# Kernel optimization log

Hardware: AMD Instinct MI355X
Metric: run time of the kernel (lower is better)

## Reference

```python
import jax, jax.numpy as jnp
import numpy as np
import math

N_NODES = 50000
N_EDGES = 800000
F_IN = 32
HID = 64


def _layernorm(x, g, b, eps=1e-5):
    mu = x.mean(-1, keepdims=True)
    var = ((x - mu) ** 2).mean(-1, keepdims=True)
    return (x - mu) / jnp.sqrt(var + eps) * g + b


def _tconv(x, src, dst, Wq, bq, Wk, bk, Wv, bv, Ws, heads):
    # PyG TransformerConv (concat=True, root_weight=True, bias=False on skip)
    N = x.shape[0]
    C = Wq.shape[1] // heads
    q = (x @ Wq + bq).reshape(N, heads, C)[dst]  # [E,H,C] gathered at targets
    k = (x @ Wk + bk).reshape(N, heads, C)[src]  # [E,H,C] gathered at sources
    v = (x @ Wv + bv).reshape(N, heads, C)[src]
    scores = (q * k).sum(-1) / math.sqrt(C)      # [E,H]
    m = jax.ops.segment_max(scores, dst, num_segments=N)   # [N,H]
    p = jnp.exp(scores - m[dst])
    denom = jax.ops.segment_sum(p, dst, num_segments=N)
    alpha = p / (denom[dst] + 1e-16)             # segment softmax over in-edges
    agg = jax.ops.segment_sum(v * alpha[..., None], dst, num_segments=N)
    return agg.reshape(N, heads * C) + x @ Ws    # + skip (no bias)


def setup_inputs() -> dict:
    key = jax.random.key(0)
    ks = iter(jax.random.split(key, 64))
    def rn(shape, s=0.1):
        return jax.random.normal(next(ks), shape, jnp.float32) * s
    inp = {
        "x": rn((N_NODES, F_IN), 1.0),
        "edge_index": jax.random.randint(next(ks), (2, N_EDGES), 0, N_NODES, dtype=jnp.int32),
        "ln0_g": jnp.ones((F_IN,), jnp.float32),
        "ln0_b": jnp.zeros((F_IN,), jnp.float32),
    }
    dims = [F_IN, HID, HID]
    for l in range(3):
        d = dims[l]
        inp[f"Wq{l}"] = rn((d, HID)); inp[f"bq{l}"] = rn((HID,), 0.05)
        inp[f"Wk{l}"] = rn((d, HID)); inp[f"bk{l}"] = rn((HID,), 0.05)
        inp[f"Wv{l}"] = rn((d, HID)); inp[f"bv{l}"] = rn((HID,), 0.05)
        inp[f"Ws{l}"] = rn((d, HID))
        inp[f"g{l}"] = jnp.ones((HID,), jnp.float32)
        inp[f"b{l}"] = jnp.zeros((HID,), jnp.float32)
    inp["Wr1"] = rn((HID, HID // 2)); inp["br1"] = jnp.zeros((HID // 2,), jnp.float32)
    inp["Wr2"] = rn((HID // 2, 1));   inp["br2"] = jnp.zeros((1,), jnp.float32)
    inp["Wt1"] = rn((HID, HID // 2)); inp["bt1"] = jnp.zeros((HID // 2,), jnp.float32)
    inp["Wt2"] = rn((HID // 2, 1));   inp["bt2"] = jnp.zeros((1,), jnp.float32)
    return inp


def reference(x, edge_index, ln0_g, ln0_b,
              Wq0, bq0, Wk0, bk0, Wv0, bv0, Ws0, g0, b0,
              Wq1, bq1, Wk1, bk1, Wv1, bv1, Ws1, g1, b1,
              Wq2, bq2, Wk2, bk2, Wv2, bv2, Ws2, g2, b2,
              Wr1, br1, Wr2, br2, Wt1, bt1, Wt2, bt2):
    src, dst = edge_index[0], edge_index[1]
    h = _layernorm(x, ln0_g, ln0_b)
    layers = [
        (Wq0, bq0, Wk0, bk0, Wv0, bv0, Ws0, g0, b0, 4),
        (Wq1, bq1, Wk1, bk1, Wv1, bv1, Ws1, g1, b1, 4),
        (Wq2, bq2, Wk2, bk2, Wv2, bv2, Ws2, g2, b2, 1),
    ]
    for i, (Wq, bq, Wk, bk, Wv, bv, Ws, g, b, heads) in enumerate(layers):
        x_res = h if h.shape[-1] == HID else None
        h = _tconv(h, src, dst, Wq, bq, Wk, bk, Wv, bv, Ws, heads)
        h = _layernorm(h, g, b)
        if x_res is not None and i > 0:
            h = h + 0.1 * x_res
        if i < len(layers) - 1:
            h = jax.nn.relu(h)  # dropout is identity in eval mode
    rtt = jax.nn.relu(h @ Wr1 + br1) @ Wr2 + br2      # [N,1]
    retrans = jax.nn.relu(h @ Wt1 + bt1) @ Wt2 + bt2  # [N,1]
    return jnp.concatenate([rtt, retrans], axis=1)    # [N,2]
```

## Files before the change

kernel.cpp:

```cpp
#include <hip/hip_runtime.h>
#include <hip/hip_bf16.h>
#include <hip/hip_fp16.h>
#include <math.h>

#define N_NODES 50000
#define N_EDGES 800000
#define HID 64
#define NBK 196
#define EPB 1024
#define SB  ((N_EDGES + EPB - 1) / EPB)
#define FLAT (NBK * SB)
#define SCAN_B ((FLAT + 255) / 256)

#define QKVS0_BLKS 3125
#define SCORE_BLKS ((N_EDGES * 4) / 256)

#define LN0_BLKS   6250
#define HIST_BLKS  SB
#define WP0_BLKS   32
#define WP12_BLKS  64
#define PREP_BLKS  (LN0_BLKS + HIST_BLKS + WP0_BLKS + 2 * WP12_BLKS)

typedef __attribute__((ext_vector_type(8))) short short8;
typedef __attribute__((ext_vector_type(4))) float float4v;
typedef __attribute__((ext_vector_type(2))) float float2v;

__device__ __forceinline__ unsigned short f32_to_bf16_rne(float f) {
    unsigned int u = __float_as_uint(f);
    unsigned int r = u + 0x7fffu + ((u >> 16) & 1u);
    return (unsigned short)(r >> 16);
}

__device__ __forceinline__ unsigned int f32_to_fp8_byte(float f) {
    return (unsigned int)__builtin_amdgcn_cvt_pk_fp8_f32(f, f, 0, false) & 0xffu;
}
template <bool HI>
__device__ __forceinline__ float2v fp8x2_to_f32(unsigned int w) {
    return __builtin_amdgcn_cvt_pk_f32_fp8((int)w, HI);
}
__device__ __forceinline__ float2 h2_to_f32(unsigned int w) {
    __half2 h = *reinterpret_cast<__half2*>(&w);
    return __half22float2(h);
}

__device__ __forceinline__ void ln0_body(int b, int t,
        const float* __restrict__ x, const float* __restrict__ g,
        const float* __restrict__ bb, float* __restrict__ h0) {
    int lane = t & 63;
    int n = b * 8 + (t >> 6) * 2 + (lane >> 5);
    int c = lane & 31;
    float v = x[n * 32 + c];
    float s = v;
    #pragma unroll
    for (int off = 1; off < 32; off <<= 1) s += __shfl_xor(s, off);
    float mu = s * (1.0f / 32.0f);
    float d = v - mu;
    float vs = d * d;
    #pragma unroll
    for (int off = 1; off < 32; off <<= 1) vs += __shfl_xor(vs, off);
    float var = vs * (1.0f / 32.0f);
    h0[n * 32 + c] = d * rsqrtf(var + 1e-5f) * g[c] + bb[c];
}

__device__ __forceinline__ void wprep_body(int idx, int KS,
        const float* __restrict__ Wq, const float* __restrict__ Wk,
        const float* __restrict__ Wv, const float* __restrict__ Ws,
        unsigned short* __restrict__ Wp) {
    int j = idx & 7;
    int lane = (idx >> 3) & 63;
    int ts = idx >> 9;
    int s = ts % KS;
    int tile = ts / KS;
    int which = tile >> 2;
    int slice = tile & 3;
    int k = s * 32 + ((lane >> 4) * 8) + j;
    int col = slice * 16 + (lane & 15);
    const float* W = (which == 0) ? Wq : (which == 1) ? Wk : (which == 2) ? Wv : Ws;
    Wp[idx] = f32_to_bf16_rne(W[k * 64 + col]);
}

__global__ __launch_bounds__(256) void prep_kernel(
        const float* __restrict__ x, const float* __restrict__ ln0g,
        const float* __restrict__ ln0b, float* __restrict__ h0,
        const int* __restrict__ dst, int* __restrict__ ghist,
        const float* __restrict__ Wq0, const float* __restrict__ Wk0,
        const float* __restrict__ Wv0, const float* __restrict__ Ws0,
        unsigned short* __restrict__ Wp0,
        const float* __restrict__ Wq1, const float* __restrict__ Wk1,
        const float* __restrict__ Wv1, const float* __restrict__ Ws1,
        unsigned short* __restrict__ Wp1,
        const float* __restrict__ Wq2, const float* __restrict__ Wk2,
        const float* __restrict__ Wv2, const float* __restrict__ Ws2,
        unsigned short* __restrict__ Wp2) {
    __shared__ int hist[NBK];
    int b = blockIdx.x;
    int t = threadIdx.x;
    if (b < LN0_BLKS) {
        ln0_body(b, t, x, ln0g, ln0b, h0);
    } else if (b < LN0_BLKS + HIST_BLKS) {
        int i = b - LN0_BLKS;
        for (int k = t; k < NBK; k += 256) hist[k] = 0;
        __syncthreads();
        int e0 = i * EPB;
        #pragma unroll
        for (int r = 0; r < EPB / 256; r++) {
            int e = e0 + r * 256 + t;
            if (e < N_EDGES) atomicAdd(&hist[dst[e] >> 8], 1);
        }
        __syncthreads();
        for (int k = t; k < NBK; k += 256) ghist[k * SB + i] = hist[k];
    } else if (b < LN0_BLKS + HIST_BLKS + WP0_BLKS) {
        int idx = (b - LN0_BLKS - HIST_BLKS) * 256 + t;
        wprep_body(idx, 1, Wq0, Wk0, Wv0, Ws0, Wp0);
    } else if (b < LN0_BLKS + HIST_BLKS + WP0_BLKS + WP12_BLKS) {
        int idx = (b - LN0_BLKS - HIST_BLKS - WP0_BLKS) * 256 + t;
        wprep_body(idx, 2, Wq1, Wk1, Wv1, Ws1, Wp1);
    } else {
        int idx = (b - LN0_BLKS - HIST_BLKS - WP0_BLKS - WP12_BLKS) * 256 + t;
        wprep_body(idx, 2, Wq2, Wk2, Wv2, Ws2, Wp2);
    }
}

__global__ void scan1_kernel(const int* __restrict__ ghist, int* __restrict__ csum) {
    int f = blockIdx.x * 256 + threadIdx.x;
    int v = (f < FLAT) ? ghist[f] : 0;
    #pragma unroll
    for (int off = 1; off < 64; off <<= 1) v += __shfl_xor(v, off);
    __shared__ int ws[4];
    if ((threadIdx.x & 63) == 0) ws[threadIdx.x >> 6] = v;
    __syncthreads();
    if (threadIdx.x == 0) csum[blockIdx.x] = ws[0] + ws[1] + ws[2] + ws[3];
}

__global__ void scan2_kernel(const int* __restrict__ csum, int* __restrict__ coff,
                             int* __restrict__ bbase, int* __restrict__ row_ptr) {
    int lane = threadIdx.x;
    int carry = 0;
    for (int base = 0; base < SCAN_B; base += 64) {
        int i = base + lane;
        int v = (i < SCAN_B) ? csum[i] : 0;
        int incl = v;
        #pragma unroll
        for (int off = 1; off < 64; off <<= 1) {
            int tt = __shfl_up(incl, off);
            if (lane >= off) incl += tt;
        }
        if (i < SCAN_B) coff[i] = carry + incl - v;
        carry += __shfl(incl, 63);
    }
    if (lane == 0) { bbase[NBK] = N_EDGES; row_ptr[N_NODES] = N_EDGES; }
}

__global__ void scan3_kernel(const int* __restrict__ ghist, const int* __restrict__ coff,
                             int* __restrict__ goff, int* __restrict__ bbase) {
    int f = blockIdx.x * 256 + threadIdx.x;
    int lane = threadIdx.x & 63;
    int w = threadIdx.x >> 6;
    int v = (f < FLAT) ? ghist[f] : 0;
    int incl = v;
    #pragma unroll
    for (int off = 1; off < 64; off <<= 1) {
        int tt = __shfl_up(incl, off);
        if (lane >= off) incl += tt;
    }
    __shared__ int ws[4];
    if (lane == 63) ws[w] = incl;
    __syncthreads();
    int woff = 0;
    #pragma unroll
    for (int k = 0; k < 4; k++) if (k < w) woff += ws[k];
    int excl = coff[blockIdx.x] + woff + incl - v;
    if (f < FLAT) {
        goff[f] = excl;
        if (f % SB == 0) bbase[f / SB] = excl;
    }
}

template <int D>
__device__ __forceinline__ void qkvs_body(int bid, int t,
        const float* __restrict__ h,
        const unsigned short* __restrict__ Wp,
        const float* __restrict__ bq, const float* __restrict__ bk,
        const float* __restrict__ bv, float scale,
        unsigned int* __restrict__ QS,
        unsigned int* __restrict__ K8, uint2* __restrict__ Vh) {
    constexpr int KS = D / 32;
    int lane = t & 63;
    int w = t >> 6;
    int n0 = bid * 16;
    int n16 = lane & 15;
    int quad = lane >> 4;
    int col = w * 16 + n16;

    short8 afrag[KS];
    #pragma unroll
    for (int s = 0; s < KS; s++) {
        const float* hp = &h[(n0 + n16) * D + s * 32 + quad * 8];
        float4 a0 = *(const float4*)hp;
        float4 a1 = *(const float4*)(hp + 4);
        short8 af;
        af[0] = (short)f32_to_bf16_rne(a0.x);
        af[1] = (short)f32_to_bf16_rne(a0.y);
        af[2] = (short)f32_to_bf16_rne(a0.z);
        af[3] = (short)f32_to_bf16_rne(a0.w);
        af[4] = (short)f32_to_bf16_rne(a1.x);
        af[5] = (short)f32_to_bf16_rne(a1.y);
        af[6] = (short)f32_to_bf16_rne(a1.z);
        af[7] = (short)f32_to_bf16_rne(a1.w);
        afrag[s] = af;
    }

    float4v accs[4];
    #pragma unroll
    for (int which = 0; which < 4; which++) {
        float4v acc = {0.0f, 0.0f, 0.0f, 0.0f};
        int tile = which * 4 + w;
        #pragma unroll
        for (int s = 0; s < KS; s++) {
            short8 bfrag = *(const short8*)&Wp[((tile * KS + s) * 64 + lane) * 8];
            acc = __builtin_amdgcn_mfma_f32_16x16x32_bf16(afrag[s], bfrag, acc, 0, 0, 0);
        }
        accs[which] = acc;
    }

    float bqc = bq[col], bkc = bk[col], bvc = bv[col];
    int j = n16 & 3;
    int mword = (col >> 2);

    #pragma unroll
    for (int r = 0; r < 4; r++) {
        int node = n0 + quad * 4 + r;
        unsigned int qw = f32_to_bf16_rne((accs[0][r] + bqc) * scale);
        unsigned int sw = f32_to_bf16_rne(accs[3][r]);
        QS[node * 64 + col] = (sw << 16) | qw;
        unsigned int ku = f32_to_fp8_byte(accs[1][r] + bkc) << (8 * j);
        ku |= __shfl_xor(ku, 1); ku |= __shfl_xor(ku, 2);
        unsigned int hb = (unsigned int)__half_as_ushort(__float2half_rn(accs[2][r] + bvc));
        unsigned int vx = (j < 2) ? (hb << (16 * j)) : 0u;
        unsigned int vy = (j >= 2) ? (hb << (16 * (j - 2))) : 0u;
        vx |= __shfl_xor(vx, 1); vx |= __shfl_xor(vx, 2);
        vy |= __shfl_xor(vy, 1); vy |= __shfl_xor(vy, 2);
        if (j == 0) {
            K8[node * 16 + mword] = ku;
            Vh[node * 16 + mword] = make_uint2(vx, vy);
        }
    }
}

template <int D>
__global__ __launch_bounds__(256) void qkvs_mfma_kernel(
        const float* __restrict__ h,
        const unsigned short* __restrict__ Wp,
        const float* __restrict__ bq, const float* __restrict__ bk,
        const float* __restrict__ bv, float scale,
        unsigned int* __restrict__ QS,
        unsigned int* __restrict__ K8, uint2* __restrict__ Vh) {
    qkvs_body<D>(blockIdx.x, threadIdx.x, h, Wp, bq, bk, bv, scale, QS, K8, Vh);
}

__global__ __launch_bounds__(256) void scatter_qkvs0_kernel(
        const int* __restrict__ src, const int* __restrict__ dst,
        const int* __restrict__ goff, int2* __restrict__ ebkt,
        const float* __restrict__ h, const unsigned short* __restrict__ Wp,
        const float* __restrict__ bq, const float* __restrict__ bk,
        const float* __restrict__ bv, float scale,
        unsigned int* __restrict__ QS,
        unsigned int* __restrict__ K8, uint2* __restrict__ Vh) {
    __shared__ int hist[NBK];
    int t = threadIdx.x;
    if (blockIdx.x < SB) {
        int i = blockIdx.x;
        for (int k = t; k < NBK; k += 256) hist[k] = 0;
        __syncthreads();
        int e0 = i * EPB;
        #pragma unroll
        for (int r = 0; r < EPB / 256; r++) {
            int e = e0 + r * 256 + t;
            if (e < N_EDGES) {
                int s = src[e], d = dst[e];
                int k = d >> 8;
                int rank = atomicAdd(&hist[k], 1);
                ebkt[goff[k * SB + i] + rank] = make_int2(s, d);
            }
        }
    } else {
        qkvs_body<32>(blockIdx.x - SB, t, h, Wp, bq, bk, bv, scale, QS, K8, Vh);
    }
}

__global__ __launch_bounds__(256) void bucket_build_kernel(
        const int2* __restrict__ ebkt, const int* __restrict__ bbase,
        int* __restrict__ row_ptr, int2* __restrict__ colb2) {
    __shared__ int ldeg[256];
    __shared__ int lcur[256];
    __shared__ int wsum[4];
    int b = blockIdx.x;
    int t = threadIdx.x;
    int cbase = bbase[b];
    int cnt = bbase[b + 1] - cbase;

    ldeg[t] = 0;
    __syncthreads();
    for (int i = t; i < cnt; i += 256) {
        int2 e = ebkt[cbase + i];
        atomicAdd(&ldeg[e.y & 255], 1);
    }
    __syncthreads();

    int lane = t & 63;
    int w = t >> 6;
    int v = ldeg[t];
    int incl = v;
    #pragma unroll
    for (int off = 1; off < 64; off <<= 1) {
        int tt = __shfl_up(incl, off);
        if (lane >= off) incl += tt;
    }
    if (lane == 63) wsum[w] = incl;
    __syncthreads();
    int woff = 0;
    #pragma unroll
    for (int k = 0; k < 4; k++) if (k < w) woff += wsum[k];
    int excl = woff + incl - v;

    int node = b * 256 + t;
    if (node < N_NODES) row_ptr[node] = cbase + excl;
    lcur[t] = excl;
    __syncthreads();

    for (int i = t; i < cnt; i += 256) {
        int2 e = ebkt[cbase + i];
        int r = atomicAdd(&lcur[e.y & 255], 1);
        colb2[cbase + r] = e;
    }
}

template <int HEADS>
__global__ __launch_bounds__(256) void score_kernel(
        const unsigned int* __restrict__ QS,
        const unsigned int* __restrict__ K8,
        const int2* __restrict__ colb2,
        float* __restrict__ p) {
    int gid = blockIdx.x * 256 + threadIdx.x;
    int e = gid >> 2;
    int slot = gid & 3;
    int2 ed = colb2[e];
    const unsigned int* qp = &QS[(size_t)ed.y * 64 + slot * 16];
    uint4 qa = *(const uint4*)qp;
    uint4 qb = *(const uint4*)(qp + 4);
    uint4 qc = *(const uint4*)(qp + 8);
    uint4 qd = *(const uint4*)(qp + 12);
    uint4 kw = *(const uint4*)&K8[(size_t)ed.x * 16 + slot * 4];

    float2v k0 = fp8x2_to_f32<false>(kw.x), k1 = fp8x2_to_f32<true>(kw.x);
    float2v k2 = fp8x2_to_f32<false>(kw.y), k3 = fp8x2_to_f32<true>(kw.y);
    float2v k4 = fp8x2_to_f32<false>(kw.z), k5 = fp8x2_to_f32<true>(kw.z);
    float2v k6 = fp8x2_to_f32<false>(kw.w), k7 = fp8x2_to_f32<true>(kw.w);

    float t;
    t =      __uint_as_float(qa.x << 16) * k0.x;
    t = fmaf(__uint_as_float(qa.y << 16), k0.y, t);
    t = fmaf(__uint_as_float(qa.z << 16), k1.x, t);
    t = fmaf(__uint_as_float(qa.w << 16), k1.y, t);
    t = fmaf(__uint_as_float(qb.x << 16), k2.x, t);
    t = fmaf(__uint_as_float(qb.y << 16), k2.y, t);
    t = fmaf(__uint_as_float(qb.z << 16), k3.x, t);
    t = fmaf(__uint_as_float(qb.w << 16), k3.y, t);
    t = fmaf(__uint_as_float(qc.x << 16), k4.x, t);
    t = fmaf(__uint_as_float(qc.y << 16), k4.y, t);
    t = fmaf(__uint_as_float(qc.z << 16), k5.x, t);
    t = fmaf(__uint_as_float(qc.w << 16), k5.y, t);
    t = fmaf(__uint_as_float(qd.x << 16), k6.x, t);
    t = fmaf(__uint_as_float(qd.y << 16), k6.y, t);
    t = fmaf(__uint_as_float(qd.z << 16), k7.x, t);
    t = fmaf(__uint_as_float(qd.w << 16), k7.y, t);

    if (HEADS == 1) {
        t += __shfl_xor(t, 1);
        t += __shfl_xor(t, 2);
    }
    float pv = __expf(t);
    if (HEADS == 4) {
        p[(size_t)e * 4 + slot] = pv;
    } else {
        if (slot == 0) p[e] = pv;
    }
}

template <int HEADS, bool RES, bool RELU, bool HEAD>
__global__ __launch_bounds__(256) void agg_kernel(
                           const unsigned int* __restrict__ QS,
                           const uint2* __restrict__ Vh,
                           const float* __restrict__ p,
                           const int2* __restrict__ colb2,
                           const int* __restrict__ row_ptr,
                           const float* __restrict__ g, const float* __restrict__ b,
                           const float* __restrict__ h_in, float* __restrict__ h_out,
                           const float* __restrict__ Wr1, const float* __restrict__ br1,
                           const float* __restrict__ Wr2, const float* __restrict__ br2,
                           const float* __restrict__ Wt1, const float* __restrict__ bt1,
                           const float* __restrict__ Wt2, const float* __restrict__ bt2,
                           float* __restrict__ out) {
    int lane = threadIdx.x & 63;
    int m = lane & 15;
    int grp = lane >> 4;
    int n = blockIdx.x * 4 + (threadIdx.x >> 6);
    int hsel = m >> 2;

    int beg = row_ptr[n], end = row_ptr[n + 1];

    float ssum = 0.0f;
    float acc0 = 0.0f, acc1 = 0.0f, acc2 = 0.0f, acc3 = 0.0f;

    for (int base = beg; base < end; base += 16) {
        #pragma unroll
        for (int c = 0; c < 4; c++) {
            int idx = base + c * 4 + grp;
            bool ok = idx < end;
            int s = 0;
            float pv = 0.0f;
            if (ok) {
                s = colb2[idx].x;
                pv = (HEADS == 4) ? p[(size_t)idx * 4 + hsel] : p[idx];
            }
            uint2 va = Vh[(size_t)s * 16 + m];
            float2 v0 = h2_to_f32(va.x), v1 = h2_to_f32(va.y);
            ssum += pv;
            acc0 = fmaf(pv, v0.x, acc0);
            acc1 = fmaf(pv, v0.y, acc1);
            acc2 = fmaf(pv, v1.x, acc2);
            acc3 = fmaf(pv, v1.y, acc3);
        }
    }

    #pragma unroll
    for (int off = 16; off < 64; off <<= 1) {
        ssum += __shfl_xor(ssum, off);
        acc0 += __shfl_xor(acc0, off);
        acc1 += __shfl_xor(acc1, off);
        acc2 += __shfl_xor(acc2, off);
        acc3 += __shfl_xor(acc3, off);
    }

    float inv = 1.0f / (ssum + 1e-16f);
    uint4 qsw = *(const uint4*)&QS[(size_t)n * 64 + 4 * m];
    float o0 = fmaf(acc0, inv, __uint_as_float(qsw.x & 0xffff0000u));
    float o1 = fmaf(acc1, inv, __uint_as_float(qsw.y & 0xffff0000u));
    float o2 = fmaf(acc2, inv, __uint_as_float(qsw.z & 0xffff0000u));
    float o3 = fmaf(acc3, inv, __uint_as_float(qsw.w & 0xffff0000u));

    float s = (o0 + o1) + (o2 + o3);
    #pragma unroll
    for (int off = 1; off < 16; off <<= 1) s += __shfl_xor(s, off);
    float mu = s * (1.0f / 64.0f);
    float d0 = o0 - mu, d1 = o1 - mu, d2 = o2 - mu, d3 = o3 - mu;
    float vs = (d0 * d0 + d1 * d1) + (d2 * d2 + d3 * d3);
    #pragma unroll
    for (int off = 1; off < 16; off <<= 1) vs += __shfl_xor(vs, off);
    float rstd = rsqrtf(vs * (1.0f / 64.0f) + 1e-5f);

    float4 gv = *(const float4*)&g[4 * m];
    float4 bv = *(const float4*)&b[4 * m];
    float y0 = d0 * rstd * gv.x + bv.x;
    float y1 = d1 * rstd * gv.y + bv.y;
    float y2 = d2 * rstd * gv.z + bv.z;
    float y3 = d3 * rstd * gv.w + bv.w;
    if (RES) {
        float4 rv = *(const float4*)&h_in[n * 64 + 4 * m];
        y0 = fmaf(0.1f, rv.x, y0);
        y1 = fmaf(0.1f, rv.y, y1);
        y2 = fmaf(0.1f, rv.z, y2);
        y3 = fmaf(0.1f, rv.w, y3);
    }
    if (RELU) {
        y0 = fmaxf(y0, 0.0f); y1 = fmaxf(y1, 0.0f);
        y2 = fmaxf(y2, 0.0f); y3 = fmaxf(y3, 0.0f);
    }

    if (!HEAD) {
        if (grp == 0) {
            float4 yv = make_float4(y0, y1, y2, y3);
            *(float4*)&h_out[n * 64 + 4 * m] = yv;
        }
    } else {
        __shared__ float sh[4][HID];
        int wave = threadIdx.x >> 6;
        if (grp == 0) {
            float4 yv = make_float4(y0, y1, y2, y3);
            *(float4*)&sh[wave][4 * m] = yv;
        }
        __syncthreads();
        int half = lane >> 5;
        int j = lane & 31;
        const float* W1 = half ? Wt1 : Wr1;
        const float* b1 = half ? bt1 : br1;
        const float* W2 = half ? Wt2 : Wr2;
        const float* b2v = half ? bt2 : br2;
        float a = b1[j];
        #pragma unroll 8
        for (int i = 0; i < 64; i++) a = fmaf(sh[wave][i], W1[i * 32 + j], a);
        a = fmaxf(a, 0.0f);
        float r = a * W2[j];
        #pragma unroll
        for (int off = 1; off < 32; off <<= 1) r += __shfl_xor(r, off);
        if (j == 0) out[n * 2 + half] = r + b2v[0];
    }
}

extern "C" void kernel_launch(void* const* d_in, const int* in_sizes, int n_in,
                              void* d_out, int out_size, void* d_ws, size_t ws_size,
                              hipStream_t stream) {
    const float* x    = (const float*)d_in[0];
    const int*   ei   = (const int*)d_in[1];
    const int*   src  = ei;
    const int*   dst  = ei + N_EDGES;
    const float* ln0g = (const float*)d_in[2];
    const float* ln0b = (const float*)d_in[3];

    const float* P[27];
    for (int i = 0; i < 27; i++) P[i] = (const float*)d_in[4 + i];
    const float* Wr1 = (const float*)d_in[31];
    const float* br1 = (const float*)d_in[32];
    const float* Wr2 = (const float*)d_in[33];
    const float* br2 = (const float*)d_in[34];
    const float* Wt1 = (const float*)d_in[35];
    const float* bt1 = (const float*)d_in[36];
    const float* Wt2 = (const float*)d_in[37];
    const float* bt2 = (const float*)d_in[38];

    float* out = (float*)d_out;

    float* hbuf0 = (float*)d_ws;
    float* hbuf1 = hbuf0 + N_NODES * 64;
    unsigned int* QSb = (unsigned int*)(hbuf1 + N_NODES * 64);
    unsigned int* K8 = QSb + N_NODES * 64;
    uint2* Vh    = (uint2*)(K8 + N_NODES * 16);
    float* pbuf  = (float*)(Vh + N_NODES * 16);
    int* row_ptr = (int*)(pbuf + (size_t)N_EDGES * 4);
    int2* colb2  = (int2*)(row_ptr + (N_NODES + 2));
    int* ghist   = (int*)(colb2 + N_EDGES);
    int* goff    = ghist + FLAT;
    int* csum    = goff + FLAT;
    int* coff    = csum + SCAN_B;
    int* bbase   = coff + SCAN_B;
    unsigned short* Wp0 = (unsigned short*)(bbase + NBK + 1);
    unsigned short* Wp1 = Wp0 + 16 * 1 * 512;
    unsigned short* Wp2 = Wp1 + 16 * 2 * 512;
    int2* ebkt = (int2*)hbuf1;

    prep_kernel<<<PREP_BLKS, 256, 0, stream>>>(x, ln0g, ln0b, hbuf0,
        dst, ghist,
        P[0],  P[2],  P[4],  P[6],  Wp0,
        P[9],  P[11], P[13], P[15], Wp1,
        P[18], P[20], P[22], P[24], Wp2);
    scan1_kernel<<<SCAN_B, 256, 0, stream>>>(ghist, csum);
    scan2_kernel<<<1, 64, 0, stream>>>(csum, coff, bbase, row_ptr);
    scan3_kernel<<<SCAN_B, 256, 0, stream>>>(ghist, coff, goff, bbase);
    scatter_qkvs0_kernel<<<SB + QKVS0_BLKS, 256, 0, stream>>>(src, dst, goff, ebkt,
        hbuf0, Wp0, P[1], P[3], P[5], 0.25f, QSb, K8, Vh);
    bucket_build_kernel<<<NBK, 256, 0, stream>>>(ebkt, bbase, row_ptr, colb2);

    score_kernel<4><<<SCORE_BLKS, 256, 0, stream>>>(QSb, K8, colb2, pbuf);
    agg_kernel<4, false, true, false><<<12500, 256, 0, stream>>>(QSb, Vh, pbuf,
        colb2, row_ptr, P[7], P[8], nullptr, hbuf1,
        Wr1, br1, Wr2, br2, Wt1, bt1, Wt2, bt2, out);

    qkvs_mfma_kernel<64><<<3125, 256, 0, stream>>>(hbuf1, Wp1,
        P[10], P[12], P[14], 0.25f, QSb, K8, Vh);
    score_kernel<4><<<SCORE_BLKS, 256, 0, stream>>>(QSb, K8, colb2, pbuf);
    agg_kernel<4, true, true, false><<<12500, 256, 0, stream>>>(QSb, Vh, pbuf,
        colb2, row_ptr, P[16], P[17], hbuf1, hbuf0,
        Wr1, br1, Wr2, br2, Wt1, bt1, Wt2, bt2, out);

    qkvs_mfma_kernel<64><<<3125, 256, 0, stream>>>(hbuf0, Wp2,
        P[19], P[21], P[23], 0.125f, QSb, K8, Vh);
    score_kernel<1><<<SCORE_BLKS, 256, 0, stream>>>(QSb, K8, colb2, pbuf);
    agg_kernel<1, true, false, true><<<12500, 256, 0, stream>>>(QSb, Vh, pbuf,
        colb2, row_ptr, P[25], P[26], hbuf0, hbuf1,
        Wr1, br1, Wr2, br2, Wt1, bt1, Wt2, bt2, out);
}
```

Before: 382.3 us.

## Add edge-flat block aggregation with LDS atomics and fuse score into final agg

Layers 0 and 1 now run a new flat aggregation kernel. Each block owns 32 consecutive destination nodes and walks their combined CSR edge range, accumulating p*V into shared memory with atomics, then applies LayerNorm, residual and ReLU. This is meant to remove per-node load imbalance and idle lanes on low-degree nodes. For the single-head last layer, the separate score kernel is dropped and the attention logits are computed inside agg_kernel from K8 and Q, which saves one kernel launch and a round trip through the p buffer. The trade-offs are LDS atomic contention in the flat kernel and extra K loads in the fused path.

```diff
diff --git a/kernel.cpp b/kernel.cpp
--- a/kernel.cpp
+++ b/kernel.cpp
@@ -14,6 +14,9 @@
 
 #define QKVS0_BLKS 3125
 #define SCORE_BLKS ((N_EDGES * 4) / 256)
+
+#define BKF 32
+#define NBLK_FLAT ((N_NODES + BKF - 1) / BKF)
 
 #define LN0_BLKS   6250
 #define HIST_BLKS  SB
@@ -387,13 +390,110 @@
     }
 }
 
+template <bool RES>
+__global__ __launch_bounds__(256) void flat_agg_kernel(
+        const unsigned int* __restrict__ QS,
+        const uint2* __restrict__ Vh,
+        const float* __restrict__ p,
+        const int2* __restrict__ colb2,
+        const int* __restrict__ row_ptr,
+        const float* __restrict__ g, const float* __restrict__ b,
+        const float* __restrict__ h_in, float* __restrict__ h_out) {
+    __shared__ float shAcc[BKF][HID];
+    __shared__ float shSum[BKF][4];
+    int t = threadIdx.x;
+    int n0 = blockIdx.x * BKF;
+
+    for (int i = t; i < BKF * HID; i += 256) ((float*)shAcc)[i] = 0.0f;
+    for (int i = t; i < BKF * 4; i += 256) ((float*)shSum)[i] = 0.0f;
+    __syncthreads();
+
+    int lane = t & 63;
+    int wid = t >> 6;
+    int m = lane & 15;
+    int eg = lane >> 4;
+    int hsel = m >> 2;
+
+    int ebeg = row_ptr[n0];
+    int eend = row_ptr[min(n0 + BKF, N_NODES)];
+
+    int eb = ebeg + wid * 4;
+    int eA = eb + eg;
+    bool okA = eA < eend;
+    int2 sdA = okA ? colb2[eA] : make_int2(0, n0);
+    float pA = okA ? p[(size_t)eA * 4 + hsel] : 0.0f;
+
+    for (; eb < eend; eb += 16) {
+        uint2 vh = Vh[(size_t)sdA.x * 16 + m];
+        int eB = eb + 16 + eg;
+        bool okB = eB < eend;
+        int2 sdB = okB ? colb2[eB] : make_int2(0, n0);
+        float pB = okB ? p[(size_t)eB * 4 + hsel] : 0.0f;
+
+        int ln = sdA.y - n0;
+        float2 v0 = h2_to_f32(vh.x), v1 = h2_to_f32(vh.y);
+        atomicAdd(&shAcc[ln][4 * m + 0], pA * v0.x);
+        atomicAdd(&shAcc[ln][4 * m + 1], pA * v0.y);
+        atomicAdd(&shAcc[ln][4 * m + 2], pA * v1.x);
+        atomicAdd(&shAcc[ln][4 * m + 3], pA * v1.y);
+        if ((m & 3) == 0) atomicAdd(&shSum[ln][hsel], pA);
+
+        sdA = sdB; pA = pB;
+    }
+    __syncthreads();
+
+    int grp = lane >> 4;
+    #pragma unroll
+    for (int pp = 0; pp < 2; pp++) {
+        int ln = pp * 16 + wid * 4 + grp;
+        int n = n0 + ln;
+        if (n < N_NODES) {
+            float4 av = *(float4*)&shAcc[ln][4 * m];
+            float ssum = shSum[ln][hsel];
+            float inv = 1.0f / (ssum + 1e-16f);
+            uint4 qsw = *(const uint4*)&QS[(size_t)n * 64 + 4 * m];
+            float o0 = fmaf(av.x, inv, __uint_as_float(qsw.x & 0xffff0000u));
+            float o1 = fmaf(av.y, inv, __uint_as_float(qsw.y & 0xffff0000u));
+            float o2 = fmaf(av.z, inv, __uint_as_float(qsw.z & 0xffff0000u));
+            float o3 = fmaf(av.w, inv, __uint_as_float(qsw.w & 0xffff0000u));
+
+            float s = (o0 + o1) + (o2 + o3);
+            #pragma unroll
+            for (int off = 1; off < 16; off <<= 1) s += __shfl_xor(s, off);
+            float mu = s * (1.0f / 64.0f);
+            float d0 = o0 - mu, d1 = o1 - mu, d2 = o2 - mu, d3 = o3 - mu;
+            float vs = (d0 * d0 + d1 * d1) + (d2 * d2 + d3 * d3);
+            #pragma unroll
+            for (int off = 1; off < 16; off <<= 1) vs += __shfl_xor(vs, off);
+            float rstd = rsqrtf(vs * (1.0f / 64.0f) + 1e-5f);
+
+            float4 gv = *(const float4*)&g[4 * m];
+            float4 bv = *(const float4*)&b[4 * m];
+            float y0 = d0 * rstd * gv.x + bv.x;
+            float y1 = d1 * rstd * gv.y + bv.y;
+            float y2 = d2 * rstd * gv.z + bv.z;
+            float y3 = d3 * rstd * gv.w + bv.w;
+            if (RES) {
+                float4 rv = *(const float4*)&h_in[(size_t)n * 64 + 4 * m];
+                y0 = fmaf(0.1f, rv.x, y0);
+                y1 = fmaf(0.1f, rv.y, y1);
+                y2 = fmaf(0.1f, rv.z, y2);
+                y3 = fmaf(0.1f, rv.w, y3);
+            }
+            y0 = fmaxf(y0, 0.0f); y1 = fmaxf(y1, 0.0f);
+            y2 = fmaxf(y2, 0.0f); y3 = fmaxf(y3, 0.0f);
+            float4 yv = make_float4(y0, y1, y2, y3);
+            *(float4*)&h_out[(size_t)n * 64 + 4 * m] = yv;
+        }
+    }
+}
+
 template <int HEADS, bool RES, bool RELU, bool HEAD>
 __global__ __launch_bounds__(256) void agg_kernel(
                            const unsigned int* __restrict__ QS,
+                           const unsigned int* __restrict__ K8,
                            const uint2* __restrict__ Vh,
-                           const float* __restrict__ p,
-                           const int2* __restrict__ colb2,
-                           const int* __restrict__ row_ptr,
+                           const int* __restrict__ row_ptr, const int2* __restrict__ colb2,
                            const float* __restrict__ g, const float* __restrict__ b,
                            const float* __restrict__ h_in, float* __restrict__ h_out,
                            const float* __restrict__ Wr1, const float* __restrict__ br1,
@@ -401,35 +501,79 @@
                            const float* __restrict__ Wt1, const float* __restrict__ bt1,
                            const float* __restrict__ Wt2, const float* __restrict__ bt2,
                            float* __restrict__ out) {
+    constexpr int C = HID / HEADS;
     int lane = threadIdx.x & 63;
     int m = lane & 15;
     int grp = lane >> 4;
     int n = blockIdx.x * 4 + (threadIdx.x >> 6);
-    int hsel = m >> 2;
+
+    uint4 qsw = *(const uint4*)&QS[(size_t)n * 64 + 4 * m];
+    float4 q4 = make_float4(__uint_as_float(qsw.x << 16),
+                            __uint_as_float(qsw.y << 16),
+                            __uint_as_float(qsw.z << 16),
+                            __uint_as_float(qsw.w << 16));
 
     int beg = row_ptr[n], end = row_ptr[n + 1];
 
     float ssum = 0.0f;
     float acc0 = 0.0f, acc1 = 0.0f, acc2 = 0.0f, acc3 = 0.0f;
 
-    for (int base = beg; base < end; base += 16) {
-        #pragma unroll
-        for (int c = 0; c < 4; c++) {
-            int idx = base + c * 4 + grp;
-            bool ok = idx < end;
-            int s = 0;
-            float pv = 0.0f;
-            if (ok) {
-                s = colb2[idx].x;
-                pv = (HEADS == 4) ? p[(size_t)idx * 4 + hsel] : p[idx];
+    for (int base = beg; base < end; base += 64) {
+        int limit = min(end - base, 64);
+        int src_l = (base + lane < end) ? colb2[base + lane].x : 0;
+        for (int sub = 0; sub < limit; sub += 16) {
+            int e0 = sub + grp, e1 = sub + 4 + grp, e2 = sub + 8 + grp, e3 = sub + 12 + grp;
+            int s0 = __shfl(src_l, e0);
+            int s1 = __shfl(src_l, e1);
+            int s2 = __shfl(src_l, e2);
+            int s3 = __shfl(src_l, e3);
+            bool v0ok = e0 < limit, v1ok = e1 < limit, v2ok = e2 < limit, v3ok = e3 < limit;
+            unsigned int ka0 = 0, ka1 = 0, ka2 = 0, ka3 = 0;
+            uint2 va0 = make_uint2(0, 0), va1 = va0, va2 = va0, va3 = va0;
+            if (v0ok) { ka0 = K8[(size_t)s0 * 16 + m]; va0 = Vh[(size_t)s0 * 16 + m]; }
+            if (v1ok) { ka1 = K8[(size_t)s1 * 16 + m]; va1 = Vh[(size_t)s1 * 16 + m]; }
+            if (v2ok) { ka2 = K8[(size_t)s2 * 16 + m]; va2 = Vh[(size_t)s2 * 16 + m]; }
+            if (v3ok) { ka3 = K8[(size_t)s3 * 16 + m]; va3 = Vh[(size_t)s3 * 16 + m]; }
+
+            float2v k0a = fp8x2_to_f32<false>(ka0), k0b = fp8x2_to_f32<true>(ka0);
+            float2v k1a = fp8x2_to_f32<false>(ka1), k1b = fp8x2_to_f32<true>(ka1);
+            float2v k2a = fp8x2_to_f32<false>(ka2), k2b = fp8x2_to_f32<true>(ka2);
+            float2v k3a = fp8x2_to_f32<false>(ka3), k3b = fp8x2_to_f32<true>(ka3);
+
+            float t0 = fmaf(q4.x, k0a.x, fmaf(q4.y, k0a.y,
+                       fmaf(q4.z, k0b.x, q4.w * k0b.y)));
+            float t1 = fmaf(q4.x, k1a.x, fmaf(q4.y, k1a.y,
+                       fmaf(q4.z, k1b.x, q4.w * k1b.y)));
+            float t2 = fmaf(q4.x, k2a.x, fmaf(q4.y, k2a.y,
+                       fmaf(q4.z, k2b.x, q4.w * k2b.y)));
+            float t3 = fmaf(q4.x, k3a.x, fmaf(q4.y, k3a.y,
+                       fmaf(q4.z, k3b.x, q4.w * k3b.y)));
+            #pragma unroll
+            for (int off = 1; off < C / 4; off <<= 1) {
+                t0 += __shfl_xor(t0, off);
+                t1 += __shfl_xor(t1, off);
+                t2 += __shfl_xor(t2, off);
+                t3 += __shfl_xor(t3, off);
             }
-            uint2 va = Vh[(size_t)s * 16 + m];
-            float2 v0 = h2_to_f32(va.x), v1 = h2_to_f32(va.y);
-            ssum += pv;
-            acc0 = fmaf(pv, v0.x, acc0);
-            acc1 = fmaf(pv, v0.y, acc1);
-            acc2 = fmaf(pv, v1.x, acc2);
-            acc3 = fmaf(pv, v1.y, acc3);
+            float p0 = v0ok ? __expf(t0) : 0.0f;
+            float p1 = v1ok ? __expf(t1) : 0.0f;
+            float p2 = v2ok ? __expf(t2) : 0.0f;
+            float p3 = v3ok ? __expf(t3) : 0.0f;
+            ssum += (p0 + p1) + (p2 + p3);
+
+            float2 v0a = h2_to_f32(va0.x), v0b = h2_to_f32(va0.y);
+            float2 v1a = h2_to_f32(va1.x), v1b = h2_to_f32(va1.y);
+            float2 v2a = h2_to_f32(va2.x), v2b = h2_to_f32(va2.y);
+            float2 v3a = h2_to_f32(va3.x), v3b = h2_to_f32(va3.y);
+
+            acc0 = fmaf(p0, v0a.x, fmaf(p1, v1a.x,
+                   fmaf(p2, v2a.x, fmaf(p3, v3a.x, acc0))));
+            acc1 = fmaf(p0, v0a.y, fmaf(p1, v1a.y,
+                   fmaf(p2, v2a.y, fmaf(p3, v3a.y, acc1))));
+            acc2 = fmaf(p0, v0b.x, fmaf(p1, v1b.x,
+                   fmaf(p2, v2b.x, fmaf(p3, v3b.x, acc2))));
+            acc3 = fmaf(p0, v0b.y, fmaf(p1, v1b.y,
+                   fmaf(p2, v2b.y, fmaf(p3, v3b.y, acc3))));
         }
     }
 
@@ -443,7 +587,6 @@
     }
 
     float inv = 1.0f / (ssum + 1e-16f);
-    uint4 qsw = *(const uint4*)&QS[(size_t)n * 64 + 4 * m];
     float o0 = fmaf(acc0, inv, __uint_as_float(qsw.x & 0xffff0000u));
     float o1 = fmaf(acc1, inv, __uint_as_float(qsw.y & 0xffff0000u));
     float o2 = fmaf(acc2, inv, __uint_as_float(qsw.z & 0xffff0000u));
@@ -466,7 +609,7 @@
     float y2 = d2 * rstd * gv.z + bv.z;
     float y3 = d3 * rstd * gv.w + bv.w;
     if (RES) {
-        float4 rv = *(const float4*)&h_in[n * 64 + 4 * m];
+        float4 rv = *(const float4*)&h_in[(size_t)n * 64 + 4 * m];
         y0 = fmaf(0.1f, rv.x, y0);
         y1 = fmaf(0.1f, rv.y, y1);
         y2 = fmaf(0.1f, rv.z, y2);
@@ -480,7 +623,7 @@
     if (!HEAD) {
         if (grp == 0) {
             float4 yv = make_float4(y0, y1, y2, y3);
-            *(float4*)&h_out[n * 64 + 4 * m] = yv;
+            *(float4*)&h_out[(size_t)n * 64 + 4 * m] = yv;
         }
     } else {
         __shared__ float sh[4][HID];
@@ -561,21 +704,18 @@
     bucket_build_kernel<<<NBK, 256, 0, stream>>>(ebkt, bbase, row_ptr, colb2);
 
     score_kernel<4><<<SCORE_BLKS, 256, 0, stream>>>(QSb, K8, colb2, pbuf);
-    agg_kernel<4, false, true, false><<<12500, 256, 0, stream>>>(QSb, Vh, pbuf,
-        colb2, row_ptr, P[7], P[8], nullptr, hbuf1,
-        Wr1, br1, Wr2, br2, Wt1, bt1, Wt2, bt2, out);
+    flat_agg_kernel<false><<<NBLK_FLAT, 256, 0, stream>>>(QSb, Vh, pbuf,
+        colb2, row_ptr, P[7], P[8], nullptr, hbuf1);
 
     qkvs_mfma_kernel<64><<<3125, 256, 0, stream>>>(hbuf1, Wp1,
         P[10], P[12], P[14], 0.25f, QSb, K8, Vh);
     score_kernel<4><<<SCORE_BLKS, 256, 0, stream>>>(QSb, K8, colb2, pbuf);
-    agg_kernel<4, true, true, false><<<12500, 256, 0, stream>>>(QSb, Vh, pbuf,
-        colb2, row_ptr, P[16], P[17], hbuf1, hbuf0,
-        Wr1, br1, Wr2, br2, Wt1, bt1, Wt2, bt2, out);
+    flat_agg_kernel<true><<<NBLK_FLAT, 256, 0, stream>>>(QSb, Vh, pbuf,
+        colb2, row_ptr, P[16], P[17], hbuf1, hbuf0);
 
     qkvs_mfma_kernel<64><<<3125, 256, 0, stream>>>(hbuf0, Wp2,
         P[19], P[21], P[23], 0.125f, QSb, K8, Vh);
-    score_kernel<1><<<SCORE_BLKS, 256, 0, stream>>>(QSb, K8, colb2, pbuf);
-    agg_kernel<1, true, false, true><<<12500, 256, 0, stream>>>(QSb, Vh, pbuf,
-        colb2, row_ptr, P[25], P[26], hbuf0, hbuf1,
+    agg_kernel<1, true, false, true><<<12500, 256, 0, stream>>>(QSb, K8, Vh,
+        row_ptr, colb2, P[25], P[26], hbuf0, hbuf1,
         Wr1, br1, Wr2, br2, Wt1, bt1, Wt2, bt2, out);
 }
```

After: 942.2 us. +146.4%, slower.
